# Kernel tuning notes

Hardware: AMD Instinct MI355X
Metric: run time of the kernel (lower is better)

The kernel has to match this reference:

```python
import jax, jax.numpy as jnp
import numpy as np

B, N, M, D, NHEAD, FF, C, K = 2, 16384, 2048, 256, 8, 512, 50, 3
HID = 128          # embed/pos hidden
HEAD_HID = 256     # seg head hidden
L = 4              # depth
EPS = 1e-5


def setup_inputs() -> dict:
    key = jax.random.key(0)
    ks = jax.random.split(key, 32)
    g = lambda i, shape: jax.random.normal(ks[i], shape, dtype=jnp.float32) * 0.02
    z = lambda shape: jnp.zeros(shape, jnp.float32)
    o = lambda shape: jnp.ones(shape, jnp.float32)
    return {
        "xyz": jax.random.normal(ks[0], (B, N, 3), dtype=jnp.float32),
        "embed_w1": g(1, (3, HID)), "embed_b1": z((HID,)),
        "embed_w2": g(2, (HID, D)), "embed_b2": z((D,)),
        "pos_w1": g(3, (3, HID)), "pos_b1": z((HID,)),
        "pos_w2": g(4, (HID, D)), "pos_b2": z((D,)),
        "Wq": g(5, (L, D, D)), "bq": z((L, D)),
        "Wk": g(6, (L, D, D)), "bk": z((L, D)),
        "Wv": g(7, (L, D, D)), "bv": z((L, D)),
        "Wo": g(8, (L, D, D)), "bo": z((L, D)),
        "ln1_s": o((L, D)), "ln1_b": z((L, D)),
        "W1": g(9, (L, D, FF)), "b1": z((L, FF)),
        "W2": g(10, (L, FF, D)), "b2": z((L, D)),
        "ln2_s": o((L, D)), "ln2_b": z((L, D)),
        "head_w1": g(11, (D, HEAD_HID)), "head_b1": z((HEAD_HID,)),
        "head_w2": g(12, (HEAD_HID, C)), "head_b2": z((C,)),
    }


def _ln(x, s, b):
    m = x.mean(-1, keepdims=True)
    v = ((x - m) ** 2).mean(-1, keepdims=True)
    return (x - m) / jnp.sqrt(v + EPS) * s + b


def reference(xyz, embed_w1, embed_b1, embed_w2, embed_b2,
              pos_w1, pos_b1, pos_w2, pos_b2,
              Wq, bq, Wk, bk, Wv, bv, Wo, bo, ln1_s, ln1_b,
              W1, b1, W2, b2, ln2_s, ln2_b,
              head_w1, head_b1, head_w2, head_b2):
    # deterministic token subsample (replaces randperm stub): strided pick of M points
    stride = N // M
    tok = xyz[:, ::stride, :][:, :M]                                  # [B,M,3]
    # per-point embed + learned positional encoding
    x = jax.nn.relu(tok @ embed_w1 + embed_b1) @ embed_w2 + embed_b2  # [B,M,D]
    x = x + jax.nn.relu(tok @ pos_w1 + pos_b1) @ pos_w2 + pos_b2
    dh = D // NHEAD
    scale = 1.0 / jnp.sqrt(jnp.float32(dh))

    def layer(x, p):
        wq, bq_, wk, bk_, wv, bv_, wo, bo_, l1s, l1b, w1, b1_, w2, b2_, l2s, l2b = p
        # pre-norm MHSA
        y = _ln(x, l1s, l1b)
        q = (y @ wq + bq_).reshape(B, M, NHEAD, dh)
        k = (y @ wk + bk_).reshape(B, M, NHEAD, dh)
        v = (y @ wv + bv_).reshape(B, M, NHEAD, dh)
        att = jax.nn.softmax(jnp.einsum('bqhd,bkhd->bhqk', q, k) * scale, axis=-1)
        o = jnp.einsum('bhqk,bkhd->bqhd', att, v).reshape(B, M, D)
        x = x + o @ wo + bo_
        # pre-norm FFN (gelu, exact erf as in torch)
        y = _ln(x, l2s, l2b)
        x = x + jax.nn.gelu(y @ w1 + b1_, approximate=False) @ w2 + b2_
        return x, None

    x, _ = jax.lax.scan(layer, x, (Wq, bq, Wk, bk, Wv, bv, Wo, bo,
                                   ln1_s, ln1_b, W1, b1, W2, b2, ln2_s, ln2_b))
    logits_tok = jax.nn.relu(x @ head_w1 + head_b1) @ head_w2 + head_b2  # [B,M,C]

    # kNN propagation N->M: dist^2 = |q|^2 + |k|^2 - 2 q.k, topk smallest
    q2 = (xyz ** 2).sum(-1)[..., None]            # [B,N,1]
    k2 = (tok ** 2).sum(-1)[:, None, :]           # [B,1,M]
    dist = q2 + k2 - 2.0 * jnp.einsum('bnd,bmd->bnm', xyz, tok)
    dist = jax.lax.stop_gradient(jnp.maximum(dist, 0.0))
    idx = jax.lax.top_k(-dist, K)[1]              # [B,N,K]
    logits_nk = logits_tok[jnp.arange(B)[:, None, None], idx]  # [B,N,K,C]
    return logits_nk.mean(axis=2)                 # [B,N,C]
```

## Files before the change

kernel.cpp:

```cpp
#include <hip/hip_runtime.h>
#include <hip/hip_bf16.h>
#include <math.h>

#define B_ 2
#define N_ 16384
#define M_ 2048
#define D_ 256
#define NHEAD_ 8
#define DH_ 32
#define FF_ 512
#define C_ 50
#define HID_ 128
#define HHID_ 256
#define L_ 4
#define EPS_ 1e-5f
#define TOK_ (B_*M_)
#define QSCALE_ 0.25507604155757994f

typedef short short8 __attribute__((ext_vector_type(8)));
typedef short short4_t __attribute__((ext_vector_type(4)));
typedef float f32x4 __attribute__((ext_vector_type(4)));

__device__ __forceinline__ short f2bf(float f) {
  union { float f; unsigned u; } c; c.f = f;
  unsigned u = c.u;
  unsigned r = (u + 0x7FFFu + ((u >> 16) & 1u)) >> 16;
  return (short)r;
}
__device__ __forceinline__ float fast_exp2(float x) {
  float r;
  asm("v_exp_f32 %0, %1" : "=v"(r) : "v"(x));
  return r;
}
__device__ __forceinline__ unsigned cvt_pk_bf16(float lo, float hi) {
  unsigned r;
  asm("v_cvt_pk_bf16_f32 %0, %1, %2" : "=v"(r) : "v"(lo), "v"(hi));
  return r;
}

__global__ __launch_bounds__(256) void wconv_all(
    const float* __restrict__ Wq, const float* __restrict__ Wk,
    const float* __restrict__ Wv, const float* __restrict__ Wo,
    const float* __restrict__ W1, const float* __restrict__ W2,
    const float* __restrict__ h1,
    short* __restrict__ WqT, short* __restrict__ WkT,
    short* __restrict__ WvT, short* __restrict__ WoT,
    short* __restrict__ W1T, short* __restrict__ W2T, short* __restrict__ h1T) {
  int bid = blockIdx.x;
  const float* W; short* WT; int Kd, Nd, tn, tk;
  if (bid < 256) {
    int mat = bid >> 6, rem = bid & 63, l = rem >> 4, t = rem & 15;
    W  = (mat == 0 ? Wq : mat == 1 ? Wk : mat == 2 ? Wv : Wo) + l * 65536;
    WT = (mat == 0 ? WqT : mat == 1 ? WkT : mat == 2 ? WvT : WoT) + l * 65536;
    Kd = 256; Nd = 256; tn = t & 3; tk = t >> 2;
  } else if (bid < 384) {
    int rem = bid - 256, l = rem >> 5, t = rem & 31;
    W = W1 + l * 131072; WT = W1T + l * 131072;
    Kd = 256; Nd = 512; tn = t & 7; tk = t >> 3;
  } else if (bid < 512) {
    int rem = bid - 384, l = rem >> 5, t = rem & 31;
    W = W2 + l * 131072; WT = W2T + l * 131072;
    Kd = 512; Nd = 256; tn = t & 3; tk = t >> 2;
  } else {
    int t = bid - 512;
    W = h1; WT = h1T; Kd = 256; Nd = 256; tn = t & 3; tk = t >> 2;
  }
  int n0 = tn * 64, k0 = tk * 64;
  __shared__ short ts[64][72];
  int tid = threadIdx.x;
  #pragma unroll
  for (int i = 0; i < 4; ++i) {
    int r = i * 16 + (tid >> 4);
    int c4 = (tid & 15) * 4;
    float4 v = *(const float4*)&W[(size_t)(k0 + r) * Nd + n0 + c4];
    ts[c4 + 0][r] = f2bf(v.x);
    ts[c4 + 1][r] = f2bf(v.y);
    ts[c4 + 2][r] = f2bf(v.z);
    ts[c4 + 3][r] = f2bf(v.w);
  }
  __syncthreads();
  #pragma unroll
  for (int i = 0; i < 2; ++i) {
    int n = i * 32 + (tid >> 3);
    int kc = (tid & 7) * 8;
    *(short8*)&WT[(size_t)(n0 + n) * Kd + k0 + kc] = *(short8*)&ts[n][kc];
  }
}

__global__ __launch_bounds__(128) void embed_kernel(
    const float* __restrict__ xyz,
    const float* __restrict__ ew1, const float* __restrict__ eb1,
    const float* __restrict__ ew2, const float* __restrict__ eb2,
    const float* __restrict__ pw1, const float* __restrict__ pb1,
    const float* __restrict__ pw2, const float* __restrict__ pb2,
    float* __restrict__ x) {
  int t = blockIdx.x;
  int b = t / M_, m = t % M_;
  const float* p = xyz + ((size_t)b * N_ + (size_t)m * 8) * 3;
  float t0 = p[0], t1 = p[1], t2 = p[2];
  __shared__ float he[HID_], hp[HID_];
  int j = threadIdx.x;
  {
    float a = fmaf(t0, ew1[j], fmaf(t1, ew1[HID_ + j], fmaf(t2, ew1[2 * HID_ + j], eb1[j])));
    he[j] = fmaxf(a, 0.f);
    float c = fmaf(t0, pw1[j], fmaf(t1, pw1[HID_ + j], fmaf(t2, pw1[2 * HID_ + j], pb1[j])));
    hp[j] = fmaxf(c, 0.f);
  }
  __syncthreads();
  for (int d = j; d < D_; d += HID_) {
    float acc = eb2[d] + pb2[d];
    for (int k = 0; k < HID_; ++k) {
      acc = fmaf(he[k], ew2[k * D_ + d], acc);
      acc = fmaf(hp[k], pw2[k * D_ + d], acc);
    }
    x[(size_t)t * D_ + d] = acc;
  }
}

__global__ __launch_bounds__(256) void ln_kernel(
    const float* __restrict__ x, const float* __restrict__ s,
    const float* __restrict__ bb, short* __restrict__ y16) {
  int r = blockIdx.x * 4 + (threadIdx.x >> 6);
  int t = threadIdx.x & 63;
  const float4* xr = (const float4*)(x + (size_t)r * D_);
  float4 v = xr[t];
  float sum = v.x + v.y + v.z + v.w;
  #pragma unroll
  for (int o = 1; o < 64; o <<= 1) sum += __shfl_xor(sum, o, 64);
  float mean = sum * (1.f / D_);
  float dx = v.x - mean, dy = v.y - mean, dz = v.z - mean, dw = v.w - mean;
  float vs = dx * dx + dy * dy + dz * dz + dw * dw;
  #pragma unroll
  for (int o = 1; o < 64; o <<= 1) vs += __shfl_xor(vs, o, 64);
  float inv = 1.0f / sqrtf(vs * (1.f / D_) + EPS_);
  float4 sv = ((const float4*)s)[t];
  float4 bv = ((const float4*)bb)[t];
  short4_t ov;
  ov[0] = f2bf(dx * inv * sv.x + bv.x);
  ov[1] = f2bf(dy * inv * sv.y + bv.y);
  ov[2] = f2bf(dz * inv * sv.z + bv.z);
  ov[3] = f2bf(dw * inv * sv.w + bv.w);
  *(short4_t*)(y16 + (size_t)r * D_ + t * 4) = ov;
}

__global__ __launch_bounds__(256) void head2_kernel(
    const float* __restrict__ y, const float* __restrict__ w2,
    const float* __restrict__ b2, float* __restrict__ lt) {
  __shared__ float ys[4][HHID_];
  int w = threadIdx.x >> 6, l = threadIdx.x & 63;
  int t = blockIdx.x * 4 + w;
  float4 v = ((const float4*)(y + (size_t)t * HHID_))[l];
  *(float4*)&ys[w][l * 4] = v;
  int c = l < C_ ? l : 0;
  float a0 = 0.f, a1 = 0.f, a2 = 0.f, a3 = 0.f;
  #pragma unroll 4
  for (int k = 0; k < HHID_; k += 4) {
    a0 = fmaf(ys[w][k + 0], w2[(k + 0) * C_ + c], a0);
    a1 = fmaf(ys[w][k + 1], w2[(k + 1) * C_ + c], a1);
    a2 = fmaf(ys[w][k + 2], w2[(k + 2) * C_ + c], a2);
    a3 = fmaf(ys[w][k + 3], w2[(k + 3) * C_ + c], a3);
  }
  if (l < C_) lt[(size_t)t * C_ + l] = (a0 + a1) + (a2 + a3) + b2[l];
}

template <int ACT, int RES>
__device__ __forceinline__ void gemm16_body(
    const short* __restrict__ A16, const short* __restrict__ WT,
    const float* __restrict__ bias, const float* __restrict__ R,
    float* __restrict__ C, short* __restrict__ C16, float oscale,
    int K, int Ncols, int m0, int n0) {
  __shared__ short As[64][40];
  __shared__ short Bs[64][40];
  int tid = threadIdx.x;
  int w = tid >> 6, l = tid & 63;
  int lq = l & 15, lg = l >> 4;
  int wr = (w & 1) * 32, wc = (w >> 1) * 32;
  int sr = tid >> 2, sk = (tid & 3) * 8;
  f32x4 acc00 = {0.f, 0.f, 0.f, 0.f};
  f32x4 acc01 = {0.f, 0.f, 0.f, 0.f};
  f32x4 acc10 = {0.f, 0.f, 0.f, 0.f};
  f32x4 acc11 = {0.f, 0.f, 0.f, 0.f};
  for (int kk = 0; kk < K; kk += 32) {
    __syncthreads();
    *(short8*)&As[sr][sk] = *(const short8*)&A16[(size_t)(m0 + sr) * K + kk + sk];
    *(short8*)&Bs[sr][sk] = *(const short8*)&WT[(size_t)(n0 + sr) * K + kk + sk];
    __syncthreads();
    short8 a0 = *(short8*)&As[wr + lq][lg * 8];
    short8 a1 = *(short8*)&As[wr + 16 + lq][lg * 8];
    short8 b0 = *(short8*)&Bs[wc + lq][lg * 8];
    short8 b1 = *(short8*)&Bs[wc + 16 + lq][lg * 8];
    acc00 = __builtin_amdgcn_mfma_f32_16x16x32_bf16(a0, b0, acc00, 0, 0, 0);
    acc01 = __builtin_amdgcn_mfma_f32_16x16x32_bf16(a0, b1, acc01, 0, 0, 0);
    acc10 = __builtin_amdgcn_mfma_f32_16x16x32_bf16(a1, b0, acc10, 0, 0, 0);
    acc11 = __builtin_amdgcn_mfma_f32_16x16x32_bf16(a1, b1, acc11, 0, 0, 0);
  }
  #pragma unroll
  for (int fi = 0; fi < 2; ++fi) {
    int row = m0 + wr + fi * 16 + lg * 4;
    #pragma unroll
    for (int r = 0; r < 4; ++r) {
      #pragma unroll
      for (int fj = 0; fj < 2; ++fj) {
        int col = n0 + wc + fj * 16 + lq;
        float v = (fi == 0 ? (fj == 0 ? acc00[r] : acc01[r])
                           : (fj == 0 ? acc10[r] : acc11[r])) + bias[col];
        if (ACT == 1) v = fmaxf(v, 0.f);
        else if (ACT == 2) v = 0.5f * v * (1.f + erff(v * 0.70710678118654752f));
        if (RES) v += R[(size_t)(row + r) * Ncols + col];
        if (C)   C[(size_t)(row + r) * Ncols + col] = v;
        if (C16) C16[(size_t)(row + r) * Ncols + col] = f2bf(v * oscale);
      }
    }
  }
}

template <int ACT, int RES>
__global__ __launch_bounds__(256) void gemm16(
    const short* __restrict__ A16, const short* __restrict__ WT,
    const float* __restrict__ bias, const float* __restrict__ R,
    float* __restrict__ C, short* __restrict__ C16,
    int K, int Ncols) {
  gemm16_body<ACT, RES>(A16, WT, bias, R, C, C16, 1.f, K, Ncols,
                        blockIdx.y * 64, blockIdx.x * 64);
}

__global__ __launch_bounds__(256) void qkv16(
    const short* __restrict__ A16,
    const short* __restrict__ WqT, const short* __restrict__ WkT, const short* __restrict__ WvT,
    const float* __restrict__ bq, const float* __restrict__ bk, const float* __restrict__ bv,
    short* __restrict__ q16, short* __restrict__ k16, short* __restrict__ v16) {
  int sel = blockIdx.x >> 2;
  int n0 = (blockIdx.x & 3) << 6;
  const short* WT = sel == 0 ? WqT : (sel == 1 ? WkT : WvT);
  const float* bb = sel == 0 ? bq : (sel == 1 ? bk : bv);
  short* out16 = sel == 0 ? q16 : (sel == 1 ? k16 : v16);
  float oscale = sel == 0 ? QSCALE_ : 1.f;
  gemm16_body<0, 0>(A16, WT, bb, nullptr, nullptr, out16, oscale, D_, D_,
                    blockIdx.y * 64, n0);
}

__global__ __launch_bounds__(256) void vtrans_kernel(
    const short* __restrict__ v16, short* __restrict__ vt16) {
  int bid = blockIdx.x;
  int mt = bid & 31;
  int h = (bid >> 5) & 7;
  int b = bid >> 8;
  __shared__ short ts[64][40];
  int m0 = mt * 64;
  int tid = threadIdx.x;
  int mm = tid >> 2, dd = (tid & 3) * 8;
  *(short8*)&ts[mm][dd] =
      *(const short8*)&v16[(size_t)(b * M_ + m0 + mm) * D_ + h * DH_ + dd];
  __syncthreads();
  int d = tid >> 3, mc = (tid & 7) * 8;
  short8 r;
  #pragma unroll
  for (int j = 0; j < 8; ++j) r[j] = ts[mc + j][d];
  *(short8*)&vt16[(size_t)((b * NHEAD_ + h) * DH_ + d) * M_ + m0 + mc] = r;
}

#define KSTR 40
#define VSTR 72
#define PSTR 72
__global__ __launch_bounds__(256) void attn_mfma_kernel(
    const short* __restrict__ q16, const short* __restrict__ k16,
    const short* __restrict__ vt16,
    float* __restrict__ po0, float* __restrict__ po1,
    float* __restrict__ po2, float* __restrict__ po3,
    float* __restrict__ pl) {
  __shared__ short Ks[64][KSTR];
  __shared__ short Vt[32][VSTR];
  __shared__ short Ps[4][16][PSTR];
  int bid = blockIdx.x;
  int quar = bid & 3;
  int qt = (bid >> 2) & 31;
  int h  = (bid >> 7) & 7;
  int b  = bid >> 10;
  int tid = threadIdx.x;
  int w  = tid >> 6;
  int l  = tid & 63;
  int lq = l & 15;
  int lg = l >> 4;

  short8 qf = *(const short8*)&q16[(size_t)(b * M_ + qt * 64 + w * 16 + lq) * D_ + h * DH_ + lg * 8];

  float l_i = 0.f;
  f32x4 o0 = {0.f, 0.f, 0.f, 0.f};
  f32x4 o1 = {0.f, 0.f, 0.f, 0.f};
  int srow = tid >> 2, scol = (tid & 3) * 8;
  int vd = tid >> 3, vm = (tid & 7) * 8;
  const short* kp = k16 + (size_t)(b * M_ + quar * 512 + srow) * D_ + h * DH_ + scol;
  const short* vp = vt16 + (size_t)((b * NHEAD_ + h) * DH_ + vd) * M_ + quar * 512 + vm;

  for (int kt = 0; kt < 8; ++kt) {
    __syncthreads();
    *(short8*)&Ks[srow][scol] = *(const short8*)(kp + (size_t)(kt * 64) * D_);
    *(short8*)&Vt[vd][vm]     = *(const short8*)(vp + kt * 64);
    __syncthreads();
    f32x4 st[4];
    #pragma unroll
    for (int t = 0; t < 4; ++t) {
      short8 kf = *(short8*)&Ks[t * 16 + lq][lg * 8];
      f32x4 z = {0.f, 0.f, 0.f, 0.f};
      st[t] = __builtin_amdgcn_mfma_f32_16x16x32_bf16(kf, qf, z, 0, 0, 0);
    }
    #pragma unroll
    for (int t = 0; t < 4; ++t)
      #pragma unroll
      for (int r2 = 0; r2 < 4; ++r2) {
        st[t][r2] = fast_exp2(st[t][r2]);
        l_i += st[t][r2];
      }
    {
      unsigned* pw = (unsigned*)&Ps[w][lq][0];
      #pragma unroll
      for (int t = 0; t < 4; ++t) {
        uint2 pk;
        pk.x = cvt_pk_bf16(st[t][0], st[t][1]);
        pk.y = cvt_pk_bf16(st[t][2], st[t][3]);
        *(uint2*)(pw + t * 8 + lg * 2) = pk;
      }
    }
    #pragma unroll
    for (int c = 0; c < 2; ++c) {
      short8 pf = *(short8*)&Ps[w][lq][c * 32 + lg * 8];
      short8 v0 = *(short8*)&Vt[lq][c * 32 + lg * 8];
      short8 v1 = *(short8*)&Vt[16 + lq][c * 32 + lg * 8];
      o0 = __builtin_amdgcn_mfma_f32_16x16x32_bf16(v0, pf, o0, 0, 0, 0);
      o1 = __builtin_amdgcn_mfma_f32_16x16x32_bf16(v1, pf, o1, 0, 0, 0);
    }
  }
  l_i += __shfl_xor(l_i, 16, 64);
  l_i += __shfl_xor(l_i, 32, 64);
  int f = (b * NHEAD_ + h) * M_ + qt * 64 + w * 16 + lq;
  float* pp = (quar == 0 ? po0 : quar == 1 ? po1 : quar == 2 ? po2 : po3) + (size_t)f * 32;
  #pragma unroll
  for (int r2 = 0; r2 < 4; ++r2) pp[lg * 4 + r2] = o0[r2];
  #pragma unroll
  for (int r2 = 0; r2 < 4; ++r2) pp[16 + lg * 4 + r2] = o1[r2];
  if (lg == 0) pl[quar * (16 * M_) + f] = l_i;
}

__global__ __launch_bounds__(256) void attn_combine(
    const float* __restrict__ po0, const float* __restrict__ po1,
    const float* __restrict__ po2, const float* __restrict__ po3,
    const float* __restrict__ pl, short* __restrict__ ob16) {
  int idx = blockIdx.x * 256 + threadIdx.x;
  int f = idx >> 3, dq = (idx & 7) * 4;
  float inv = 1.f / (pl[f] + pl[16 * M_ + f] + pl[32 * M_ + f] + pl[48 * M_ + f]);
  const float4 a = *(const float4*)&po0[(size_t)f * 32 + dq];
  const float4 c = *(const float4*)&po1[(size_t)f * 32 + dq];
  const float4 e = *(const float4*)&po2[(size_t)f * 32 + dq];
  const float4 g = *(const float4*)&po3[(size_t)f * 32 + dq];
  int b = f >> 14, h = (f >> 11) & 7, m = f & (M_ - 1);
  short4_t r;
  r[0] = f2bf((a.x + c.x + e.x + g.x) * inv);
  r[1] = f2bf((a.y + c.y + e.y + g.y) * inv);
  r[2] = f2bf((a.z + c.z + e.z + g.z) * inv);
  r[3] = f2bf((a.w + c.w + e.w + g.w) * inv);
  *(short4_t*)&ob16[(size_t)(b * M_ + m) * D_ + h * DH_ + dq] = r;
}

__global__ __launch_bounds__(512) void knn_kernel(
    const float* __restrict__ xyz, const float* __restrict__ lt,
    float* __restrict__ out) {
  __shared__ float4 tok[2064];
  int b = blockIdx.x >> 9;
  int q0 = (blockIdx.x & 511) << 5;
  int tid = threadIdx.x;
  for (int i = tid; i < M_; i += 512) {
    const float* tp = xyz + ((size_t)b * N_ + (size_t)i * 8) * 3;
    float a = tp[0], bb = tp[1], cc = tp[2];
    tok[i + (i >> 7)] = make_float4(a, bb, cc, a * a + bb * bb + cc * cc);
  }
  __syncthreads();
  int g = tid >> 4, sl = tid & 15;
  int n = q0 + g;
  const float* qp = xyz + ((size_t)b * N_ + n) * 3;
  float qx = qp[0], qy = qp[1], qz = qp[2];
  float q2 = qx * qx + qy * qy + qz * qz;
  float dd0 = INFINITY, dd1 = INFINITY, dd2 = INFINITY;
  int ii0 = 0, ii1 = 0, ii2 = 0;
  const float4* cp = &tok[sl * 129];
  int mb = sl << 7;
  #pragma unroll 2
  for (int j = 0; j < 128; ++j) {
    float4 t = cp[j];
    float dot = fmaf(qx, t.x, fmaf(qy, t.y, qz * t.z));
    float d = fmaxf(q2 + t.w - 2.f * dot, 0.f);
    if (d < dd2) {
      int m = mb + j;
      if (d < dd1) {
        dd2 = dd1; ii2 = ii1;
        if (d < dd0) { dd1 = dd0; ii1 = ii0; dd0 = d; ii0 = m; }
        else         { dd1 = d;  ii1 = m; }
      } else         { dd2 = d;  ii2 = m; }
    }
  }
  auto insT = [&](float d, int i) {
    if (d < dd2 || (d == dd2 && i < ii2)) {
      if (d < dd1 || (d == dd1 && i < ii1)) {
        dd2 = dd1; ii2 = ii1;
        if (d < dd0 || (d == dd0 && i < ii0)) { dd1 = dd0; ii1 = ii0; dd0 = d; ii0 = i; }
        else { dd1 = d; ii1 = i; }
      } else { dd2 = d; ii2 = i; }
    }
  };
  #pragma unroll
  for (int off = 1; off < 16; off <<= 1) {
    float p0 = __shfl_xor(dd0, off, 64); int pi0 = __shfl_xor(ii0, off, 64);
    float p1 = __shfl_xor(dd1, off, 64); int pi1 = __shfl_xor(ii1, off, 64);
    float p2 = __shfl_xor(dd2, off, 64); int pi2 = __shfl_xor(ii2, off, 64);
    insT(p0, pi0); insT(p1, pi1); insT(p2, pi2);
  }
  const float* l0 = lt + ((size_t)b * M_ + ii0) * C_;
  const float* l1 = lt + ((size_t)b * M_ + ii1) * C_;
  const float* l2 = lt + ((size_t)b * M_ + ii2) * C_;
  float* op = out + ((size_t)b * N_ + n) * C_;
  for (int cc = sl; cc < C_; cc += 16)
    op[cc] = (l0[cc] + l1[cc] + l2[cc]) * (1.f / 3.f);
}

extern "C" void kernel_launch(void* const* d_in, const int* in_sizes, int n_in,
                              void* d_out, int out_size, void* d_ws, size_t ws_size,
                              hipStream_t stream) {
  const float* xyz  = (const float*)d_in[0];
  const float* ew1  = (const float*)d_in[1];
  const float* eb1  = (const float*)d_in[2];
  const float* ew2  = (const float*)d_in[3];
  const float* eb2  = (const float*)d_in[4];
  const float* pw1  = (const float*)d_in[5];
  const float* pb1  = (const float*)d_in[6];
  const float* pw2  = (const float*)d_in[7];
  const float* pb2  = (const float*)d_in[8];
  const float* Wq   = (const float*)d_in[9];
  const float* bq   = (const float*)d_in[10];
  const float* Wk   = (const float*)d_in[11];
  const float* bk   = (const float*)d_in[12];
  const float* Wv   = (const float*)d_in[13];
  const float* bv   = (const float*)d_in[14];
  const float* Wo   = (const float*)d_in[15];
  const float* bo   = (const float*)d_in[16];
  const float* ln1s = (const float*)d_in[17];
  const float* ln1b = (const float*)d_in[18];
  const float* W1   = (const float*)d_in[19];
  const float* b1   = (const float*)d_in[20];
  const float* W2   = (const float*)d_in[21];
  const float* b2   = (const float*)d_in[22];
  const float* ln2s = (const float*)d_in[23];
  const float* ln2b = (const float*)d_in[24];
  const float* hw1  = (const float*)d_in[25];
  const float* hb1  = (const float*)d_in[26];
  const float* hw2  = (const float*)d_in[27];
  const float* hb2  = (const float*)d_in[28];
  float* out = (float*)d_out;

  float* x   = (float*)d_ws;
  float* y   = x + 1048576;
  float* po2 = y + 1048576;
  float* po3 = po2 + 1048576;
  float* lt  = po3 + 1048576;
  short* y16 = (short*)(lt + 204800);
  short* q16 = y16 + 1048576;
  short* k16 = q16 + 1048576;
  short* v16 = k16 + 1048576;
  short* vt16 = v16 + 1048576;
  short* ob16 = vt16 + 1048576;
  short* x16  = ob16 + 1048576;
  short* ff16 = x16 + 1048576;
  short* WqT = ff16 + 2097152;
  short* WkT = WqT + 262144;
  short* WvT = WkT + 262144;
  short* WoT = WvT + 262144;
  short* W1T = WoT + 262144;
  short* W2T = W1T + 524288;
  short* h1T = W2T + 524288;
  float* po0 = y;
  float* po1 = (float*)ff16;
  float* pl  = lt;

  wconv_all<<<528, 256, 0, stream>>>(Wq, Wk, Wv, Wo, W1, W2, hw1,
                                     WqT, WkT, WvT, WoT, W1T, W2T, h1T);
  embed_kernel<<<TOK_, 128, 0, stream>>>(xyz, ew1, eb1, ew2, eb2, pw1, pb1, pw2, pb2, x);

  dim3 gQKV(12, TOK_ / 64);
  dim3 gD(D_ / 64, TOK_ / 64);
  dim3 gF(FF_ / 64, TOK_ / 64);
  for (int l = 0; l < L_; ++l) {
    ln_kernel<<<TOK_ / 4, 256, 0, stream>>>(x, ln1s + l * D_, ln1b + l * D_, y16);
    qkv16<<<gQKV, 256, 0, stream>>>(y16, WqT + l * 65536, WkT + l * 65536, WvT + l * 65536,
                                    bq + l * D_, bk + l * D_, bv + l * D_, q16, k16, v16);
    vtrans_kernel<<<512, 256, 0, stream>>>(v16, vt16);
    attn_mfma_kernel<<<2048, 256, 0, stream>>>(q16, k16, vt16, po0, po1, po2, po3, pl);
    attn_combine<<<1024, 256, 0, stream>>>(po0, po1, po2, po3, pl, ob16);
    gemm16<0, 1><<<gD, 256, 0, stream>>>(ob16, WoT + l * 65536, bo + l * D_, x, x, nullptr, D_, D_);
    ln_kernel<<<TOK_ / 4, 256, 0, stream>>>(x, ln2s + l * D_, ln2b + l * D_, y16);
    gemm16<2, 0><<<gF, 256, 0, stream>>>(y16, W1T + l * 131072, b1 + l * FF_, nullptr, nullptr, ff16, D_, FF_);
    gemm16<0, 1><<<gD, 256, 0, stream>>>(ff16, W2T + l * 131072, b2 + l * D_, x, x, x16, FF_, D_);
  }
  gemm16<1, 0><<<gD, 256, 0, stream>>>(x16, h1T, hb1, nullptr, y, nullptr, D_, HHID_);
  head2_kernel<<<TOK_ / 4, 256, 0, stream>>>(y, hw2, hb2, lt);
  knn_kernel<<<1024, 512, 0, stream>>>(xyz, lt, out);
}
```

Baseline: 402.5 us.

## Fuse V transpose into QKV, attn combine into Wo GEMM, two-pass kNN

The V projection now writes its transposed layout straight from the GEMM epilogue, so the separate transpose kernel goes away. Combining the partial attention outputs now happens inside a new Wo GEMM that builds its A tile in LDS, removing the attn_combine launch and the round trip through ob16. kNN is now two passes: a branch-free med3-based top-3 distance pass finds a threshold, and a second pass collects indices with tie-breaking. This trades fewer launches and less memory traffic for redundant combine work across the four column blocks of wo_gemm and a doubled distance loop in kNN.

```diff
diff --git a/kernel.cpp b/kernel.cpp
--- a/kernel.cpp
+++ b/kernel.cpp
@@ -35,6 +35,11 @@
 __device__ __forceinline__ unsigned cvt_pk_bf16(float lo, float hi) {
   unsigned r;
   asm("v_cvt_pk_bf16_f32 %0, %1, %2" : "=v"(r) : "v"(lo), "v"(hi));
+  return r;
+}
+__device__ __forceinline__ float med3f(float a, float b, float c) {
+  float r;
+  asm("v_med3_f32 %0, %1, %2, %3" : "=v"(r) : "v"(a), "v"(b), "v"(c));
   return r;
 }
 
@@ -167,8 +172,8 @@
 __device__ __forceinline__ void gemm16_body(
     const short* __restrict__ A16, const short* __restrict__ WT,
     const float* __restrict__ bias, const float* __restrict__ R,
-    float* __restrict__ C, short* __restrict__ C16, float oscale,
-    int K, int Ncols, int m0, int n0) {
+    float* __restrict__ C, short* __restrict__ C16, short* __restrict__ VT,
+    float oscale, int K, int Ncols, int m0, int n0) {
   __shared__ short As[64][40];
   __shared__ short Bs[64][40];
   int tid = threadIdx.x;
@@ -198,10 +203,11 @@
   for (int fi = 0; fi < 2; ++fi) {
     int row = m0 + wr + fi * 16 + lg * 4;
     #pragma unroll
-    for (int r = 0; r < 4; ++r) {
+    for (int fj = 0; fj < 2; ++fj) {
+      int col = n0 + wc + fj * 16 + lq;
+      short4_t vt4;
       #pragma unroll
-      for (int fj = 0; fj < 2; ++fj) {
-        int col = n0 + wc + fj * 16 + lq;
+      for (int r = 0; r < 4; ++r) {
         float v = (fi == 0 ? (fj == 0 ? acc00[r] : acc01[r])
                            : (fj == 0 ? acc10[r] : acc11[r])) + bias[col];
         if (ACT == 1) v = fmaxf(v, 0.f);
@@ -209,6 +215,11 @@
         if (RES) v += R[(size_t)(row + r) * Ncols + col];
         if (C)   C[(size_t)(row + r) * Ncols + col] = v;
         if (C16) C16[(size_t)(row + r) * Ncols + col] = f2bf(v * oscale);
+        if (VT)  vt4[r] = f2bf(v);
+      }
+      if (VT) {
+        int bb = row >> 11, mm = row & (M_ - 1);
+        *(short4_t*)&VT[((size_t)(bb * 256 + col)) * M_ + mm] = vt4;
       }
     }
   }
@@ -220,7 +231,7 @@
     const float* __restrict__ bias, const float* __restrict__ R,
     float* __restrict__ C, short* __restrict__ C16,
     int K, int Ncols) {
-  gemm16_body<ACT, RES>(A16, WT, bias, R, C, C16, 1.f, K, Ncols,
+  gemm16_body<ACT, RES>(A16, WT, bias, R, C, C16, nullptr, 1.f, K, Ncols,
                         blockIdx.y * 64, blockIdx.x * 64);
 }
 
@@ -228,35 +239,83 @@
     const short* __restrict__ A16,
     const short* __restrict__ WqT, const short* __restrict__ WkT, const short* __restrict__ WvT,
     const float* __restrict__ bq, const float* __restrict__ bk, const float* __restrict__ bv,
-    short* __restrict__ q16, short* __restrict__ k16, short* __restrict__ v16) {
+    short* __restrict__ q16, short* __restrict__ k16, short* __restrict__ vt16) {
   int sel = blockIdx.x >> 2;
   int n0 = (blockIdx.x & 3) << 6;
-  const short* WT = sel == 0 ? WqT : (sel == 1 ? WkT : WvT);
-  const float* bb = sel == 0 ? bq : (sel == 1 ? bk : bv);
-  short* out16 = sel == 0 ? q16 : (sel == 1 ? k16 : v16);
-  float oscale = sel == 0 ? QSCALE_ : 1.f;
-  gemm16_body<0, 0>(A16, WT, bb, nullptr, nullptr, out16, oscale, D_, D_,
-                    blockIdx.y * 64, n0);
-}
-
-__global__ __launch_bounds__(256) void vtrans_kernel(
-    const short* __restrict__ v16, short* __restrict__ vt16) {
-  int bid = blockIdx.x;
-  int mt = bid & 31;
-  int h = (bid >> 5) & 7;
-  int b = bid >> 8;
-  __shared__ short ts[64][40];
-  int m0 = mt * 64;
+  int m0 = blockIdx.y * 64;
+  if (sel == 0) {
+    gemm16_body<0, 0>(A16, WqT, bq, nullptr, nullptr, q16, nullptr, QSCALE_, D_, D_, m0, n0);
+  } else if (sel == 1) {
+    gemm16_body<0, 0>(A16, WkT, bk, nullptr, nullptr, k16, nullptr, 1.f, D_, D_, m0, n0);
+  } else {
+    gemm16_body<0, 0>(A16, WvT, bv, nullptr, nullptr, nullptr, vt16, 1.f, D_, D_, m0, n0);
+  }
+}
+
+__global__ __launch_bounds__(256) void wo_gemm(
+    const float* __restrict__ po0, const float* __restrict__ po1,
+    const float* __restrict__ po2, const float* __restrict__ po3,
+    const float* __restrict__ pl, const short* __restrict__ WT,
+    const float* __restrict__ bias, float* __restrict__ X) {
+  __shared__ short As[64][260];
+  __shared__ short Bs[64][40];
   int tid = threadIdx.x;
-  int mm = tid >> 2, dd = (tid & 3) * 8;
-  *(short8*)&ts[mm][dd] =
-      *(const short8*)&v16[(size_t)(b * M_ + m0 + mm) * D_ + h * DH_ + dd];
-  __syncthreads();
-  int d = tid >> 3, mc = (tid & 7) * 8;
-  short8 r;
-  #pragma unroll
-  for (int j = 0; j < 8; ++j) r[j] = ts[mc + j][d];
-  *(short8*)&vt16[(size_t)((b * NHEAD_ + h) * DH_ + d) * M_ + m0 + mc] = r;
+  int w = tid >> 6, l = tid & 63;
+  int m0 = blockIdx.y * 64, n0 = blockIdx.x * 64;
+  #pragma unroll 4
+  for (int c = 0; c < 16; ++c) {
+    int t = w * 16 + c;
+    int row = m0 + t;
+    int bb = row >> 11, mm = row & (M_ - 1);
+    int h = l >> 3, d0 = (l & 7) * 4;
+    size_t f = (size_t)(bb * NHEAD_ + h) * M_ + mm;
+    float inv = 1.f / (pl[f] + pl[16 * M_ + f] + pl[32 * M_ + f] + pl[48 * M_ + f]);
+    float4 p0 = *(const float4*)&po0[f * 32 + d0];
+    float4 p1 = *(const float4*)&po1[f * 32 + d0];
+    float4 p2 = *(const float4*)&po2[f * 32 + d0];
+    float4 p3 = *(const float4*)&po3[f * 32 + d0];
+    short4_t s;
+    s[0] = f2bf((p0.x + p1.x + p2.x + p3.x) * inv);
+    s[1] = f2bf((p0.y + p1.y + p2.y + p3.y) * inv);
+    s[2] = f2bf((p0.z + p1.z + p2.z + p3.z) * inv);
+    s[3] = f2bf((p0.w + p1.w + p2.w + p3.w) * inv);
+    *(short4_t*)&As[t][l * 4] = s;
+  }
+  int lq = l & 15, lg = l >> 4;
+  int wr = (w & 1) * 32, wc = (w >> 1) * 32;
+  int sr = tid >> 2, sk = (tid & 3) * 8;
+  f32x4 acc00 = {0.f, 0.f, 0.f, 0.f};
+  f32x4 acc01 = {0.f, 0.f, 0.f, 0.f};
+  f32x4 acc10 = {0.f, 0.f, 0.f, 0.f};
+  f32x4 acc11 = {0.f, 0.f, 0.f, 0.f};
+  for (int kk = 0; kk < D_; kk += 32) {
+    __syncthreads();
+    *(short8*)&Bs[sr][sk] = *(const short8*)&WT[(size_t)(n0 + sr) * D_ + kk + sk];
+    __syncthreads();
+    short8 a0 = *(short8*)&As[wr + lq][kk + lg * 8];
+    short8 a1 = *(short8*)&As[wr + 16 + lq][kk + lg * 8];
+    short8 b0 = *(short8*)&Bs[wc + lq][lg * 8];
+    short8 b1 = *(short8*)&Bs[wc + 16 + lq][lg * 8];
+    acc00 = __builtin_amdgcn_mfma_f32_16x16x32_bf16(a0, b0, acc00, 0, 0, 0);
+    acc01 = __builtin_amdgcn_mfma_f32_16x16x32_bf16(a0, b1, acc01, 0, 0, 0);
+    acc10 = __builtin_amdgcn_mfma_f32_16x16x32_bf16(a1, b0, acc10, 0, 0, 0);
+    acc11 = __builtin_amdgcn_mfma_f32_16x16x32_bf16(a1, b1, acc11, 0, 0, 0);
+  }
+  #pragma unroll
+  for (int fi = 0; fi < 2; ++fi) {
+    int row = m0 + wr + fi * 16 + lg * 4;
+    #pragma unroll
+    for (int fj = 0; fj < 2; ++fj) {
+      int col = n0 + wc + fj * 16 + lq;
+      #pragma unroll
+      for (int r = 0; r < 4; ++r) {
+        float v = (fi == 0 ? (fj == 0 ? acc00[r] : acc01[r])
+                           : (fj == 0 ? acc10[r] : acc11[r])) + bias[col];
+        v += X[(size_t)(row + r) * D_ + col];
+        X[(size_t)(row + r) * D_ + col] = v;
+      }
+    }
+  }
 }
 
 #define KSTR 40
@@ -341,26 +400,6 @@
   if (lg == 0) pl[quar * (16 * M_) + f] = l_i;
 }
 
-__global__ __launch_bounds__(256) void attn_combine(
-    const float* __restrict__ po0, const float* __restrict__ po1,
-    const float* __restrict__ po2, const float* __restrict__ po3,
-    const float* __restrict__ pl, short* __restrict__ ob16) {
-  int idx = blockIdx.x * 256 + threadIdx.x;
-  int f = idx >> 3, dq = (idx & 7) * 4;
-  float inv = 1.f / (pl[f] + pl[16 * M_ + f] + pl[32 * M_ + f] + pl[48 * M_ + f]);
-  const float4 a = *(const float4*)&po0[(size_t)f * 32 + dq];
-  const float4 c = *(const float4*)&po1[(size_t)f * 32 + dq];
-  const float4 e = *(const float4*)&po2[(size_t)f * 32 + dq];
-  const float4 g = *(const float4*)&po3[(size_t)f * 32 + dq];
-  int b = f >> 14, h = (f >> 11) & 7, m = f & (M_ - 1);
-  short4_t r;
-  r[0] = f2bf((a.x + c.x + e.x + g.x) * inv);
-  r[1] = f2bf((a.y + c.y + e.y + g.y) * inv);
-  r[2] = f2bf((a.z + c.z + e.z + g.z) * inv);
-  r[3] = f2bf((a.w + c.w + e.w + g.w) * inv);
-  *(short4_t*)&ob16[(size_t)(b * M_ + m) * D_ + h * DH_ + dq] = r;
-}
-
 __global__ __launch_bounds__(512) void knn_kernel(
     const float* __restrict__ xyz, const float* __restrict__ lt,
     float* __restrict__ out) {
@@ -379,43 +418,61 @@
   const float* qp = xyz + ((size_t)b * N_ + n) * 3;
   float qx = qp[0], qy = qp[1], qz = qp[2];
   float q2 = qx * qx + qy * qy + qz * qz;
+  const float4* cp = &tok[sl * 129];
   float dd0 = INFINITY, dd1 = INFINITY, dd2 = INFINITY;
-  int ii0 = 0, ii1 = 0, ii2 = 0;
-  const float4* cp = &tok[sl * 129];
-  int mb = sl << 7;
-  #pragma unroll 2
+  #pragma unroll 4
   for (int j = 0; j < 128; ++j) {
     float4 t = cp[j];
     float dot = fmaf(qx, t.x, fmaf(qy, t.y, qz * t.z));
     float d = fmaxf(q2 + t.w - 2.f * dot, 0.f);
-    if (d < dd2) {
-      int m = mb + j;
-      if (d < dd1) {
-        dd2 = dd1; ii2 = ii1;
-        if (d < dd0) { dd1 = dd0; ii1 = ii0; dd0 = d; ii0 = m; }
-        else         { dd1 = d;  ii1 = m; }
-      } else         { dd2 = d;  ii2 = m; }
-    }
-  }
+    float n0 = fminf(dd0, d);
+    float n1 = med3f(d, dd0, dd1);
+    float n2 = med3f(d, dd1, dd2);
+    dd0 = n0; dd1 = n1; dd2 = n2;
+  }
+  #pragma unroll
+  for (int off = 1; off < 16; off <<= 1) {
+    float p0 = __shfl_xor(dd0, off, 64);
+    float p1 = __shfl_xor(dd1, off, 64);
+    float p2 = __shfl_xor(dd2, off, 64);
+    float n0, n1, n2;
+    n0 = fminf(dd0, p0); n1 = med3f(p0, dd0, dd1); n2 = med3f(p0, dd1, dd2);
+    dd0 = n0; dd1 = n1; dd2 = n2;
+    n0 = fminf(dd0, p1); n1 = med3f(p1, dd0, dd1); n2 = med3f(p1, dd1, dd2);
+    dd0 = n0; dd1 = n1; dd2 = n2;
+    n0 = fminf(dd0, p2); n1 = med3f(p2, dd0, dd1); n2 = med3f(p2, dd1, dd2);
+    dd0 = n0; dd1 = n1; dd2 = n2;
+  }
+  float thr = dd2;
+  float e0 = INFINITY, e1 = INFINITY, e2 = INFINITY;
+  int i0 = 0x7FFFFFFF, i1 = 0x7FFFFFFF, i2 = 0x7FFFFFFF;
   auto insT = [&](float d, int i) {
-    if (d < dd2 || (d == dd2 && i < ii2)) {
-      if (d < dd1 || (d == dd1 && i < ii1)) {
-        dd2 = dd1; ii2 = ii1;
-        if (d < dd0 || (d == dd0 && i < ii0)) { dd1 = dd0; ii1 = ii0; dd0 = d; ii0 = i; }
-        else { dd1 = d; ii1 = i; }
-      } else { dd2 = d; ii2 = i; }
+    if (d < e2 || (d == e2 && i < i2)) {
+      if (d < e1 || (d == e1 && i < i1)) {
+        e2 = e1; i2 = i1;
+        if (d < e0 || (d == e0 && i < i0)) { e1 = e0; i1 = i0; e0 = d; i0 = i; }
+        else { e1 = d; i1 = i; }
+      } else { e2 = d; i2 = i; }
     }
   };
+  int mb = sl << 7;
+  #pragma unroll 4
+  for (int j = 0; j < 128; ++j) {
+    float4 t = cp[j];
+    float dot = fmaf(qx, t.x, fmaf(qy, t.y, qz * t.z));
+    float d = fmaxf(q2 + t.w - 2.f * dot, 0.f);
+    if (d <= thr) insT(d, mb + j);
+  }
   #pragma unroll
   for (int off = 1; off < 16; off <<= 1) {
-    float p0 = __shfl_xor(dd0, off, 64); int pi0 = __shfl_xor(ii0, off, 64);
-    float p1 = __shfl_xor(dd1, off, 64); int pi1 = __shfl_xor(ii1, off, 64);
-    float p2 = __shfl_xor(dd2, off, 64); int pi2 = __shfl_xor(ii2, off, 64);
+    float p0 = __shfl_xor(e0, off, 64); int pi0 = __shfl_xor(i0, off, 64);
+    float p1 = __shfl_xor(e1, off, 64); int pi1 = __shfl_xor(i1, off, 64);
+    float p2 = __shfl_xor(e2, off, 64); int pi2 = __shfl_xor(i2, off, 64);
     insT(p0, pi0); insT(p1, pi1); insT(p2, pi2);
   }
-  const float* l0 = lt + ((size_t)b * M_ + ii0) * C_;
-  const float* l1 = lt + ((size_t)b * M_ + ii1) * C_;
-  const float* l2 = lt + ((size_t)b * M_ + ii2) * C_;
+  const float* l0 = lt + ((size_t)b * M_ + i0) * C_;
+  const float* l1 = lt + ((size_t)b * M_ + i1) * C_;
+  const float* l2 = lt + ((size_t)b * M_ + i2) * C_;
   float* op = out + ((size_t)b * N_ + n) * C_;
   for (int cc = sl; cc < C_; cc += 16)
     op[cc] = (l0[cc] + l1[cc] + l2[cc]) * (1.f / 3.f);
@@ -489,11 +546,9 @@
   for (int l = 0; l < L_; ++l) {
     ln_kernel<<<TOK_ / 4, 256, 0, stream>>>(x, ln1s + l * D_, ln1b + l * D_, y16);
     qkv16<<<gQKV, 256, 0, stream>>>(y16, WqT + l * 65536, WkT + l * 65536, WvT + l * 65536,
-                                    bq + l * D_, bk + l * D_, bv + l * D_, q16, k16, v16);
-    vtrans_kernel<<<512, 256, 0, stream>>>(v16, vt16);
+                                    bq + l * D_, bk + l * D_, bv + l * D_, q16, k16, vt16);
     attn_mfma_kernel<<<2048, 256, 0, stream>>>(q16, k16, vt16, po0, po1, po2, po3, pl);
-    attn_combine<<<1024, 256, 0, stream>>>(po0, po1, po2, po3, pl, ob16);
-    gemm16<0, 1><<<gD, 256, 0, stream>>>(ob16, WoT + l * 65536, bo + l * D_, x, x, nullptr, D_, D_);
+    wo_gemm<<<gD, 256, 0, stream>>>(po0, po1, po2, po3, pl, WoT + l * 65536, bo + l * D_, x);
     ln_kernel<<<TOK_ / 4, 256, 0, stream>>>(x, ln2s + l * D_, ln2b + l * D_, y16);
     gemm16<2, 0><<<gF, 256, 0, stream>>>(y16, W1T + l * 131072, b1 + l * FF_, nullptr, nullptr, ff16, D_, FF_);
     gemm16<0, 1><<<gD, 256, 0, stream>>>(ff16, W2T + l * 131072, b2 + l * D_, x, x, x16, FF_, D_);
```

New measurement: 405.2 us. About the same (+0.7%).
